# Kernel tuning notes

Hardware: AMD Instinct MI355X
Metric: run time of the kernel (lower is better)

## Reference

```python
import jax, jax.numpy as jnp
import numpy as np

H = 8                 # num_heads
SCALE = 25.0          # self.scale
SIM_THRESH = 0.75
CONF_SIM_THRESH = 0.99


def _l2n(x):
    return x / jnp.linalg.norm(x, axis=-1, keepdims=True)


def setup_inputs() -> dict:
    key = jax.random.key(0)
    ks = jax.random.split(key, 10)
    B, N1, N2, C = 1, 512, 2048, 1024
    s = 0.02
    return {
        'x_cls': jax.random.normal(ks[0], (B, N2, C), jnp.float32),
        'x_reg': jax.random.normal(ks[1], (B, N2, C), jnp.float32),
        'cls_score': jax.random.uniform(ks[2], (N2,), dtype=jnp.float32),
        'fg_score': jax.random.uniform(ks[3], (N2,), dtype=jnp.float32),
        'W_q_cls': jax.random.normal(ks[4], (C, C), jnp.float32) * s,
        'W_kv_cls': jax.random.normal(ks[5], (C, 2 * C), jnp.float32) * s,
        'W_q_reg': jax.random.normal(ks[6], (C, C), jnp.float32) * s,
        'W_kv_reg': jax.random.normal(ks[7], (C, 2 * C), jnp.float32) * s,
        'W_lin': jax.random.normal(ks[8], (2 * C, 2 * C), jnp.float32) * s,
        'b_lin': jnp.zeros((2 * C,), jnp.float32),
        'W_lin_reg': jax.random.normal(ks[9], (2 * C, 2 * C), jnp.float32) * s,
        'b_lin_reg': jnp.zeros((2 * C,), jnp.float32),
        'local_preds_num': 512,
    }


def _forward(x_cls, x_reg, cls_score, fg_score, W_q_cls, W_kv_cls, W_q_reg, W_kv_reg,
             W_lin, b_lin, W_lin_reg, b_lin_reg, N1):
    B, N2, C = x_cls.shape
    hd = C // H
    # QKV projections (torch Linear with bias=False; weights stored [in,out])
    q_cls = (x_cls[:, :N1] @ W_q_cls).reshape(B, N1, H, hd).transpose(0, 2, 1, 3)   # [B,H,N1,hd]
    kv = (x_cls @ W_kv_cls).reshape(B, N2, 2, H, hd).transpose(2, 0, 3, 1, 4)
    k_cls, v_cls = kv[0], kv[1]                                                      # [B,H,N2,hd]
    q_reg = (x_reg[:, :N1] @ W_q_reg).reshape(B, N1, H, hd).transpose(0, 2, 1, 3)
    kv = (x_reg @ W_kv_reg).reshape(B, N2, 2, H, hd).transpose(2, 0, 3, 1, 4)
    k_reg, v_reg = kv[0], kv[1]
    # L2 normalization of q, k and of v for raw similarity
    q_cls, k_cls = _l2n(q_cls), _l2n(k_cls)
    q_reg, k_reg = _l2n(q_reg), _l2n(k_reg)
    v_cls_n, v_reg_n = _l2n(v_cls), _l2n(v_reg)
    # per-key score broadcast over [1,H,N1,N2] (use_mask=False path)
    cs = cls_score.reshape(1, 1, 1, N2)
    # raw value-value similarity
    attn_cls_raw = jnp.einsum('bhqd,bhkd->bhqk', v_cls_n[:, :, :N1], v_cls_n)        # [B,H,N1,N2]
    attn_reg_raw = jnp.einsum('bhqd,bhkd->bhqk', v_reg_n[:, :, :N1], v_reg_n)
    # blended softmax attention (attn_drop=0 -> identity)
    attn_cls = jax.nn.softmax(jnp.einsum('bhqd,bhkd->bhqk', q_cls, k_cls) * SCALE * cs, axis=-1)
    attn_reg = jax.nn.softmax(jnp.einsum('bhqd,bhkd->bhqk', q_reg, k_reg) * SCALE, axis=-1)
    attn = (attn_cls + attn_reg) * 0.5
    # attended features + original local values, then output linears
    x = jnp.einsum('bhqk,bhkd->bhqd', attn, v_cls).transpose(0, 2, 1, 3).reshape(B, N1, C)
    x_ori = v_cls[:, :, :N1].transpose(0, 2, 1, 3).reshape(B, N1, C)
    out_cls = jnp.concatenate([x, x_ori], axis=-1) @ W_lin + b_lin                   # [B,N1,2C]
    xr = jnp.einsum('bhqk,bhkd->bhqd', attn, v_reg).transpose(0, 2, 1, 3).reshape(B, N1, C)
    xr_ori = v_reg[:, :, :N1].transpose(0, 2, 1, 3).reshape(B, N1, C)
    out_reg = jnp.concatenate([xr, xr_ori], axis=-1) @ W_lin_reg + b_lin_reg         # reconf=True
    # ave branch: similarity-masked renormalized second-round averaging (batch 0)
    sim_mask = (attn_cls_raw.sum(axis=1)[0] / H > SIM_THRESH).astype(x_cls.dtype)    # [N1,N2]
    obj_mask = (attn_reg_raw.sum(axis=1)[0] / H > CONF_SIM_THRESH).astype(x_cls.dtype)
    sim_round2 = jax.nn.softmax(attn.sum(axis=1)[0] / H, axis=-1)
    sim_round2 = sim_mask * sim_round2
    sim_round2 = sim_round2 / sim_round2.sum(axis=-1, keepdims=True)
    obj_w = obj_mask * sim_round2
    obj_w = obj_w / obj_w.sum(axis=-1, keepdims=True)
    support_cls = v_cls.transpose(0, 2, 1, 3).reshape(B, N2, C)[0]                   # [N2,C]
    support_reg = v_reg.transpose(0, 2, 1, 3).reshape(B, N2, C)[0]
    cls_feature = jnp.concatenate([sim_round2 @ support_cls, out_cls[0]], axis=-1)   # [N1,3C]
    reg_feature = jnp.concatenate([obj_w @ support_reg, out_reg[0]], axis=-1)        # [N1,3C]
    return cls_feature, reg_feature


def reference(x_cls, x_reg, cls_score, fg_score, W_q_cls, W_kv_cls, W_q_reg, W_kv_reg,
              W_lin, b_lin, W_lin_reg, b_lin_reg, local_preds_num):
    return _forward(x_cls, x_reg, cls_score, fg_score, W_q_cls, W_kv_cls, W_q_reg,
                    W_kv_reg, W_lin, b_lin, W_lin_reg, b_lin_reg, local_preds_num)
```

## Files before the change

kernel.cpp:

```cpp
#include <hip/hip_runtime.h>

typedef _Float16 half8 __attribute__((ext_vector_type(8)));
typedef _Float16 half4v __attribute__((ext_vector_type(4)));
typedef float f32x4 __attribute__((ext_vector_type(4)));

#define GLD16(gptr, lptr) \
    __builtin_amdgcn_global_load_lds((const __attribute__((address_space(1))) void*)(gptr), \
                                     (__attribute__((address_space(3))) void*)(lptr), 16, 0, 0)

#define WAIT_VM3   0x0F73
#define WAIT_VM0   0x0F70
#define WAIT_LGKM0 0xC07F

struct GD {
    const _Float16* A; const _Float16* B; void* C;
    const float* colScale;
    _Float16 *vnp, *vtp, *xop;
    long sAh, sAg, sBh, sBg, sSplit, sCh, sCg;
    int lda, ldb, ldc, K, SK, hmask, hshift;
    int ahx, outHalf, csMode, nx, ny, normMode;
    float alpha;
};

__global__ __launch_bounds__(512, 4)
void hgemm3(GD d0, GD d1, int zSplit)
{
    const bool second = (int)blockIdx.z >= zSplit;
    const GD& d = second ? d1 : d0;
    const int bz = second ? (int)blockIdx.z - zSplit : (int)blockIdx.z;
    const int bx = (int)blockIdx.x, by = (int)blockIdx.y;
    if (bx >= d.nx || by >= d.ny) return;

    __shared__ uint4 smem[4608];
    char* sb = (char*)smem;
    const int tid = threadIdx.x;
    const int w = tid >> 6, l = tid & 63;
    const int m0 = by << 8, n0 = bx << 7;
    const int wm = (w >> 1) << 6, wn = (w & 1) << 6;
    const int kq = l >> 4, lm = l & 15;

    const int zz = bz / d.SK, s = bz - zz * d.SK;
    const int h = d.ahx ? bx : (zz & d.hmask);
    const int g = d.ahx ? zz : (zz >> d.hshift);
    const _Float16* A = d.A + (long)h * d.sAh + (long)g * d.sAg;
    const _Float16* B = d.B + (long)h * d.sBh + (long)g * d.sBg;
    const long Coff = (long)s * d.sSplit + (long)h * d.sCh + (long)g * d.sCg;
    const int kper = d.K / d.SK, kbeg = s * kper;
    const int NT = kper >> 5;

    const int rS = (w << 4) + (l >> 2);
    const int cS = (l & 3) ^ ((l >> 3) & 3);
    const _Float16* gA0 = A + (long)(m0 + rS) * d.lda + kbeg + cS * 8;
    const _Float16* gB0 = B + (long)(n0 + rS) * d.ldb + kbeg + cS * 8;
    const int lo = w * 1024 + l * 16;

    auto stage = [&](int t) {
        char* dst = sb + (t % 3) * 24576;
        GLD16(gA0 + t * 32,                     dst + lo);
        GLD16(gA0 + (long)128 * d.lda + t * 32, dst + 8192 + lo);
        GLD16(gB0 + t * 32,                     dst + 16384 + lo);
    };

    f32x4 acc[4][4] = {};
    stage(0);
    if (NT > 1) stage(1);
    if (NT > 1) __builtin_amdgcn_s_waitcnt(WAIT_VM3);
    else        __builtin_amdgcn_s_waitcnt(WAIT_VM0);
    __builtin_amdgcn_s_barrier();

    const int sw16 = ((kq ^ ((lm >> 1) & 3)) << 4);
    for (int t = 0; t < NT; ++t) {
        const char* cb = sb + (t % 3) * 24576;
        half8 af[4], bfr[4];
        const char* pa = cb + (wm + lm) * 64 + sw16;
        const char* pb = cb + 16384 + (wn + lm) * 64 + sw16;
        #pragma unroll
        for (int i = 0; i < 4; ++i) {
            af[i]  = *(const half8*)(pa + i * 1024);
            bfr[i] = *(const half8*)(pb + i * 1024);
        }
        #pragma unroll
        for (int mi = 0; mi < 4; ++mi)
            #pragma unroll
            for (int ni = 0; ni < 4; ++ni)
                acc[mi][ni] = __builtin_amdgcn_mfma_f32_16x16x32_f16(af[mi], bfr[ni], acc[mi][ni], 0, 0, 0);
        __builtin_amdgcn_s_waitcnt(WAIT_LGKM0);
        if (t + 2 < NT) { stage(t + 2); __builtin_amdgcn_s_waitcnt(WAIT_VM3); }
        else if (t + 1 < NT) __builtin_amdgcn_s_waitcnt(WAIT_VM0);
        __builtin_amdgcn_s_barrier();
    }

    if (d.normMode == 0) {
        const int rbase = m0 + wm + kq * 4;
        #pragma unroll
        for (int mi = 0; mi < 4; ++mi) {
            #pragma unroll
            for (int ni = 0; ni < 4; ++ni) {
                const int col = n0 + wn + ni * 16 + lm;
                float cs = d.alpha;
                if (d.csMode == 1 || (d.csMode == 2 && g == 0)) cs *= d.colScale[col];
                #pragma unroll
                for (int r = 0; r < 4; ++r) {
                    const long row = rbase + mi * 16 + r;
                    const float v = acc[mi][ni][r] * cs;
                    const long off = Coff + row * d.ldc + col;
                    if (d.outHalf) ((_Float16*)d.C)[off] = (_Float16)v;
                    else           ((float*)d.C)[off] = v;
                }
            }
        }
        return;
    }

    float* part = (float*)sb;
    float ssq[4][4];
    #pragma unroll
    for (int mi = 0; mi < 4; ++mi)
        #pragma unroll
        for (int r = 0; r < 4; ++r) {
            float sq = 0.f;
            #pragma unroll
            for (int ni = 0; ni < 4; ++ni) { const float v = acc[mi][ni][r]; sq += v * v; }
            sq += __shfl_xor(sq, 1, 64);
            sq += __shfl_xor(sq, 2, 64);
            sq += __shfl_xor(sq, 4, 64);
            sq += __shfl_xor(sq, 8, 64);
            ssq[mi][r] = sq;
        }
    if (lm == 0) {
        #pragma unroll
        for (int mi = 0; mi < 4; ++mi)
            #pragma unroll
            for (int r = 0; r < 4; ++r)
                part[(w & 1) * 256 + wm + kq * 4 + mi * 16 + r] = ssq[mi][r];
    }
    __syncthreads();

    #pragma unroll
    for (int mi = 0; mi < 4; ++mi) {
        #pragma unroll
        for (int r = 0; r < 4; ++r) {
            const int rl = wm + kq * 4 + mi * 16 + r;
            const float inv = rsqrtf(part[rl] + part[256 + rl]);
            const long rg = m0 + rl;
            if (d.normMode == 1) {
                #pragma unroll
                for (int ni = 0; ni < 4; ++ni) {
                    const int col = n0 + wn + ni * 16 + lm;
                    ((_Float16*)d.C)[(long)g * 524288 + rg * 1024 + col] =
                        (_Float16)(acc[mi][ni][r] * inv);
                }
            } else if (n0 < 1024) {
                #pragma unroll
                for (int ni = 0; ni < 4; ++ni) {
                    const int col = n0 + wn + ni * 16 + lm;
                    ((_Float16*)d.C)[(long)g * 2097152 + rg * 1024 + col] =
                        (_Float16)(acc[mi][ni][r] * inv);
                }
            } else {
                #pragma unroll
                for (int ni = 0; ni < 4; ++ni) {
                    const int nL = n0 - 1024 + wn + ni * 16 + lm;
                    d.vnp[(long)g * 2097152 + rg * 1024 + nL] =
                        (_Float16)(acc[mi][ni][r] * inv);
                    if (rg < 512)
                        d.xop[((long)g * 512 + rg) * 2048 + 1024 + nL] =
                            (_Float16)acc[mi][ni][r];
                }
            }
        }
    }
    if (d.normMode == 2 && n0 >= 1024) {
        #pragma unroll
        for (int mi = 0; mi < 4; ++mi)
            #pragma unroll
            for (int ni = 0; ni < 4; ++ni) {
                const int nL = n0 - 1024 + wn + ni * 16 + lm;
                half4v t;
                t.x = (_Float16)acc[mi][ni][0]; t.y = (_Float16)acc[mi][ni][1];
                t.z = (_Float16)acc[mi][ni][2]; t.w = (_Float16)acc[mi][ni][3];
                *(half4v*)(d.vtp + (long)g * 2097152 + (long)nL * 2048
                           + m0 + wm + kq * 4 + mi * 16) = t;
            }
    }
}

static GD mkgd(const _Float16* A, const _Float16* B, void* C, const float* cscale,
               long sAh, long sAg, long sBh, long sBg, long sSplit, long sCh, long sCg,
               int lda, int ldb, int ldc, int K, int SK, int hmask, int hshift,
               int ahx, int outHalf, int csMode, int nx, int ny, float alpha)
{
    GD d; d.A=A; d.B=B; d.C=C; d.colScale=cscale;
    d.vnp=nullptr; d.vtp=nullptr; d.xop=nullptr;
    d.sAh=sAh; d.sAg=sAg; d.sBh=sBh; d.sBg=sBg; d.sSplit=sSplit; d.sCh=sCh; d.sCg=sCg;
    d.lda=lda; d.ldb=ldb; d.ldc=ldc; d.K=K; d.SK=SK; d.hmask=hmask; d.hshift=hshift;
    d.ahx=ahx; d.outHalf=outHalf; d.csMode=csMode; d.nx=nx; d.ny=ny; d.normMode=0;
    d.alpha=alpha;
    return d;
}

__global__ __launch_bounds__(256)
void prep_all(const float* __restrict__ x_cls, const float* __restrict__ x_reg,
              const float* __restrict__ Wq_c, const float* __restrict__ Wq_r,
              const float* __restrict__ Wkv_c, const float* __restrict__ Wkv_r,
              const float* __restrict__ Wl_c, const float* __restrict__ Wl_r,
              _Float16* __restrict__ xbf,
              _Float16* __restrict__ WqT, _Float16* __restrict__ WkvT,
              _Float16* __restrict__ WlinT)
{
    const int z = blockIdx.z;
    if (z == 6) {
        const int lin = blockIdx.y * 64 + blockIdx.x;
        const int which = lin >> 11;
        const int i = (lin & 2047) * 256 + threadIdx.x;
        const float* s = which ? x_reg : x_cls;
        const float4 v = ((const float4*)s)[i];
        half4v o;
        o.x = (_Float16)v.x; o.y = (_Float16)v.y; o.z = (_Float16)v.z; o.w = (_Float16)v.w;
        ((half4v*)(xbf + (size_t)which * 2097152))[i] = o;
        return;
    }
    __shared__ float t[32][33];
    const float* src; _Float16* dst; int ldsrc, lddst, nx, ky;
    switch (z) {
        case 0: src=Wq_c;  dst=WqT;            ldsrc=1024; lddst=1024; nx=32; ky=32; break;
        case 1: src=Wq_r;  dst=WqT+1048576;    ldsrc=1024; lddst=1024; nx=32; ky=32; break;
        case 2: src=Wkv_c; dst=WkvT;           ldsrc=2048; lddst=1024; nx=64; ky=32; break;
        case 3: src=Wkv_r; dst=WkvT+2097152;   ldsrc=2048; lddst=1024; nx=64; ky=32; break;
        case 4: src=Wl_c;  dst=WlinT;          ldsrc=2048; lddst=2048; nx=64; ky=64; break;
        default:src=Wl_r;  dst=WlinT+4194304;  ldsrc=2048; lddst=2048; nx=64; ky=64; break;
    }
    if ((int)blockIdx.x >= nx || (int)blockIdx.y >= ky) return;
    const int n0 = blockIdx.x << 5, k0 = blockIdx.y << 5;
    const int tx = threadIdx.x & 31, ty = threadIdx.x >> 5;
    #pragma unroll
    for (int j = ty; j < 32; j += 8)
        t[j][tx] = src[(size_t)(k0 + j) * ldsrc + n0 + tx];
    __syncthreads();
    #pragma unroll
    for (int j = ty; j < 32; j += 8)
        dst[(size_t)(n0 + j) * lddst + k0 + tx] = (_Float16)t[tx][j];
}

template<int OP>
__device__ __forceinline__ float bred(float v, float* lds)
{
    #pragma unroll
    for (int o = 32; o > 0; o >>= 1) {
        const float u = __shfl_xor(v, o, 64);
        v = OP ? fmaxf(v, u) : v + u;
    }
    __syncthreads();
    if ((threadIdx.x & 63) == 0) lds[threadIdx.x >> 6] = v;
    __syncthreads();
    return OP ? fmaxf(fmaxf(lds[0], lds[1]), fmaxf(lds[2], lds[3]))
              : lds[0] + lds[1] + lds[2] + lds[3];
}

template<int OP>
__device__ __forceinline__ void bred2(float& a, float& b, float* lds)
{
    #pragma unroll
    for (int o = 32; o > 0; o >>= 1) {
        const float ua = __shfl_xor(a, o, 64);
        const float ub = __shfl_xor(b, o, 64);
        a = OP ? fmaxf(a, ua) : a + ua;
        b = OP ? fmaxf(b, ub) : b + ub;
    }
    __syncthreads();
    if ((threadIdx.x & 63) == 0) {
        const int wi = threadIdx.x >> 6;
        lds[wi] = a; lds[4 + wi] = b;
    }
    __syncthreads();
    a = OP ? fmaxf(fmaxf(lds[0], lds[1]), fmaxf(lds[2], lds[3]))
           : lds[0] + lds[1] + lds[2] + lds[3];
    b = OP ? fmaxf(fmaxf(lds[4], lds[5]), fmaxf(lds[6], lds[7]))
           : lds[4] + lds[5] + lds[6] + lds[7];
}

__global__ __launch_bounds__(256)
void sb2_kernel(const _Float16* __restrict__ S16, const float* __restrict__ simPart,
                _Float16* __restrict__ attn,
                _Float16* __restrict__ wc, _Float16* __restrict__ wr)
{
    __shared__ float lds[8];
    const int q = blockIdx.x, t = threadIdx.x;
    const int c0 = t * 8;
    float asum[8] = {};
    for (int hh = 0; hh < 8; ++hh) {
        const size_t rb = (size_t)(hh * 512 + q) * 2048 + c0;
        const half8 hc = *(const half8*)(S16 + rb);
        const half8 hr = *(const half8*)(S16 + 8388608 + rb);
        float vc[8], vr[8];
        float mc = -1e30f, mr = -1e30f;
        #pragma unroll
        for (int j = 0; j < 8; ++j) {
            vc[j] = (float)hc[j]; vr[j] = (float)hr[j];
            mc = fmaxf(mc, vc[j]); mr = fmaxf(mr, vr[j]);
        }
        bred2<1>(mc, mr, lds);
        float sc = 0.f, sr = 0.f;
        #pragma unroll
        for (int j = 0; j < 8; ++j) {
            vc[j] = expf(vc[j] - mc); sc += vc[j];
            vr[j] = expf(vr[j] - mr); sr += vr[j];
        }
        bred2<0>(sc, sr, lds);
        const float ic = 0.5f / sc, ir = 0.5f / sr;
        half8 oa;
        #pragma unroll
        for (int j = 0; j < 8; ++j) {
            const float a = vc[j] * ic + vr[j] * ir;
            oa[j] = (_Float16)a;
            asum[j] += a;
        }
        *(half8*)(attn + rb) = oa;
    }
    float mx = -1e30f;
    #pragma unroll
    for (int j = 0; j < 8; ++j) { asum[j] *= 0.125f; mx = fmaxf(mx, asum[j]); }
    mx = bred<1>(mx, lds);
    const size_t qb = (size_t)q * 2048 + c0;
    float sim[8], reg[8];
    {
        const float4 a0 = *(const float4*)(simPart + qb);
        const float4 a1 = *(const float4*)(simPart + qb + 4);
        const float4 b0 = *(const float4*)(simPart + 2097152 + qb);
        const float4 b1 = *(const float4*)(simPart + 2097152 + qb + 4);
        sim[0]=a0.x+b0.x; sim[1]=a0.y+b0.y; sim[2]=a0.z+b0.z; sim[3]=a0.w+b0.w;
        sim[4]=a1.x+b1.x; sim[5]=a1.y+b1.y; sim[6]=a1.z+b1.z; sim[7]=a1.w+b1.w;
        const float4 c0_ = *(const float4*)(simPart + 1048576 + qb);
        const float4 c1_ = *(const float4*)(simPart + 1048576 + qb + 4);
        const float4 d0_ = *(const float4*)(simPart + 2097152 + 1048576 + qb);
        const float4 d1_ = *(const float4*)(simPart + 2097152 + 1048576 + qb + 4);
        reg[0]=c0_.x+d0_.x; reg[1]=c0_.y+d0_.y; reg[2]=c0_.z+d0_.z; reg[3]=c0_.w+d0_.w;
        reg[4]=c1_.x+d1_.x; reg[5]=c1_.y+d1_.y; reg[6]=c1_.z+d1_.z; reg[7]=c1_.w+d1_.w;
    }
    float em[8], emo[8];
    float s1 = 0.f, s2 = 0.f;
    #pragma unroll
    for (int j = 0; j < 8; ++j) {
        const float e = expf(asum[j] - mx);
        const float m  = sim[j] > 0.75f ? 1.f : 0.f;
        const float mo = reg[j] > 0.99f ? 1.f : 0.f;
        em[j] = e * m; emo[j] = e * m * mo;
        s1 += em[j]; s2 += emo[j];
    }
    bred2<0>(s1, s2, lds);
    const float i1 = 1.f / s1, i2 = 1.f / s2;
    half8 o1, o2;
    #pragma unroll
    for (int j = 0; j < 8; ++j) {
        o1[j] = (_Float16)(em[j] * i1);
        o2[j] = (_Float16)(emo[j] * i2);
    }
    *(half8*)(wc + qb) = o1;
    *(half8*)(wr + qb) = o2;
}

__global__ __launch_bounds__(256)
void build_xcat(const _Float16* __restrict__ xcatPart, _Float16* __restrict__ xcat)
{
    const int v8 = blockIdx.x * 256 + threadIdx.x;
    const int g = v8 >> 16;
    const int n = (v8 >> 7) & 511;
    const int j = (v8 & 127) * 8;
    const size_t p = (size_t)g * 524288 + (size_t)n * 1024 + j;
    float a[8] = {};
    #pragma unroll
    for (int s = 0; s < 4; ++s) {
        const half8 v = *(const half8*)(xcatPart + (size_t)s * 1048576 + p);
        #pragma unroll
        for (int k = 0; k < 8; ++k) a[k] += (float)v[k];
    }
    half8 o;
    #pragma unroll
    for (int k = 0; k < 8; ++k) o[k] = (_Float16)a[k];
    *(half8*)(xcat + ((size_t)g * 512 + n) * 2048 + j) = o;
}

__global__ __launch_bounds__(256)
void finalize(const float* __restrict__ avePart, const float* __restrict__ outPart,
              const float* __restrict__ b_lin, const float* __restrict__ b_lin_reg,
              float* __restrict__ out)
{
    const int v4 = blockIdx.x * 256 + threadIdx.x;
    const size_t base = (size_t)v4 * 4;
    const int c = (int)(base % 3072);
    const int r = (int)((base / 3072) & 511);
    const int g = (int)(base / (3072 * 512));
    float4 v;
    if (c < 1024) {
        const size_t p = (size_t)g * 524288 + (size_t)r * 1024 + c;
        v = make_float4(0.f, 0.f, 0.f, 0.f);
        #pragma unroll
        for (int s = 0; s < 4; ++s) {
            const float4 u = *(const float4*)(avePart + (size_t)s * 1048576 + p);
            v.x += u.x; v.y += u.y; v.z += u.z; v.w += u.w;
        }
    } else {
        const int cc = c - 1024;
        v = *(const float4*)((g ? b_lin_reg : b_lin) + cc);
        const size_t p = (size_t)g * 1048576 + (size_t)r * 2048 + cc;
        #pragma unroll
        for (int s = 0; s < 4; ++s) {
            const float4 u = *(const float4*)(outPart + (size_t)s * 2097152 + p);
            v.x += u.x; v.y += u.y; v.z += u.z; v.w += u.w;
        }
    }
    *(float4*)(out + base) = v;
}

extern "C" void kernel_launch(void* const* d_in, const int* in_sizes, int n_in,
                              void* d_out, int out_size, void* d_ws, size_t ws_size,
                              hipStream_t stream)
{
    const float* x_cls     = (const float*)d_in[0];
    const float* x_reg     = (const float*)d_in[1];
    const float* cls_score = (const float*)d_in[2];
    const float* W_q_cls   = (const float*)d_in[4];
    const float* W_kv_cls  = (const float*)d_in[5];
    const float* W_q_reg   = (const float*)d_in[6];
    const float* W_kv_reg  = (const float*)d_in[7];
    const float* W_lin     = (const float*)d_in[8];
    const float* b_lin     = (const float*)d_in[9];
    const float* W_lin_reg = (const float*)d_in[10];
    const float* b_lin_reg = (const float*)d_in[11];
    float* out = (float*)d_out;

    if (ws_size < (size_t)124 * 1048576) return;

    char* W = (char*)d_ws;
    auto at = [&](size_t mb) { return (void*)(W + mb * 1048576); };
    _Float16* WlinT   = (_Float16*)at(0);
    _Float16* vT      = (_Float16*)at(16);
    _Float16* w_c     = (_Float16*)at(24);
    _Float16* w_r     = (_Float16*)at(26);
    _Float16* qn      = (_Float16*)at(28);
    _Float16* kn      = (_Float16*)at(30);
    _Float16* vn      = (_Float16*)at(38);
    _Float16* xbf     = (_Float16*)at(46);
    _Float16* WkvT    = (_Float16*)at(54);
    _Float16* WqT     = (_Float16*)at(62);
    _Float16* S16     = (_Float16*)at(66);
    float*    simPart = (float*)at(46);
    _Float16* attn_h  = (_Float16*)at(28);
    float*    avePart = (float*)at(46);
    _Float16* xcatPart= (_Float16*)at(62);
    float*    outPart = (float*)at(70);
    _Float16* xcat16  = (_Float16*)at(102);

    prep_all<<<dim3(64, 64, 7), 256, 0, stream>>>(
        x_cls, x_reg, W_q_cls, W_q_reg, W_kv_cls, W_kv_reg, W_lin, W_lin_reg,
        xbf, WqT, WkvT, WlinT);

    {
        GD q  = mkgd(xbf, WqT, qn, nullptr,
                     0, 2097152, 0, 1048576, 0, 0, 0,
                     1024, 1024, 1024, 1024, 1, 0, 0, 1, 0, 0, 8, 2, 1.f);
        q.normMode = 1;
        GD kv = mkgd(xbf, WkvT, kn, nullptr,
                     0, 2097152, 0, 2097152, 0, 0, 0,
                     1024, 1024, 1024, 1024, 1, 0, 0, 1, 0, 0, 16, 8, 1.f);
        kv.normMode = 2; kv.vnp = vn; kv.vtp = vT; kv.xop = xcat16;
        hgemm3<<<dim3(16, 8, 4), 512, 0, stream>>>(q, kv, 2);
    }

    {
        GD vs = mkgd(vn, vn, simPart, nullptr,
                     0, 2097152, 0, 2097152, 2097152, 0, 1048576,
                     1024, 1024, 2048, 1024, 2, 0, 0, 0, 0, 0, 16, 2, 0.125f);
        GD sc = mkgd(qn, kn, S16, cls_score,
                     128, 524288, 128, 2097152, 0, 1048576, 8388608,
                     1024, 1024, 2048, 128, 1, 7, 3, 0, 1, 2, 16, 2, 25.f);
        hgemm3<<<dim3(16, 2, 20), 512, 0, stream>>>(vs, sc, 4);
    }

    sb2_kernel<<<512, 256, 0, stream>>>(S16, simPart, attn_h, w_c, w_r);

    {
        GD av = mkgd(attn_h, vT, xcatPart, nullptr,
                     1048576, 0, 0, 2097152, 1048576, 0, 524288,
                     2048, 2048, 1024, 2048, 4, 0, 0, 1, 1, 0, 8, 2, 1.f);
        GD ae = mkgd(w_c, vT, avePart, nullptr,
                     0, 1048576, 0, 2097152, 1048576, 0, 524288,
                     2048, 2048, 1024, 2048, 4, 0, 0, 0, 0, 0, 8, 2, 1.f);
        hgemm3<<<dim3(8, 2, 16), 512, 0, stream>>>(av, ae, 8);
    }

    build_xcat<<<512, 256, 0, stream>>>(xcatPart, xcat16);

    {
        GD ol = mkgd(xcat16, WlinT, outPart, nullptr,
                     0, 1048576, 0, 4194304, 2097152, 0, 1048576,
                     2048, 2048, 2048, 2048, 4, 0, 0, 0, 0, 0, 16, 2, 1.f);
        hgemm3<<<dim3(16, 2, 8), 512, 0, stream>>>(ol, ol, 8);
    }

    finalize<<<3072, 256, 0, stream>>>(avePart, outPart, b_lin, b_lin_reg, out);
}
```

Baseline: 271.1 us.

## Replace split-K partial buffers and finalize with atomic adds into output; drop softmax max

The split-K GEMMs for the aggregated-value and output-linear stages now atomically add their partials straight into the final output, which is pre-initialised with zeros and biases inside the prep kernel. This removes the finalize kernel and its read of the partial buffers. Separately, the softmax in sb2 drops the max-subtraction reductions, relying on bounded logits (scale 25 on normalized dot products) so that exp cannot overflow. Atomics add contention and make the summation order nondeterministic.

New measurement: 297.9 us. 9.9% more time.

```diff
diff --git a/kernel.cpp b/kernel.cpp
--- a/kernel.cpp
+++ b/kernel.cpp
@@ -18,7 +18,7 @@
     _Float16 *vnp, *vtp, *xop;
     long sAh, sAg, sBh, sBg, sSplit, sCh, sCg;
     int lda, ldb, ldc, K, SK, hmask, hshift;
-    int ahx, outHalf, csMode, nx, ny, normMode;
+    int ahx, outHalf, csMode, nx, ny, normMode, atomOut;
     float alpha;
 };
 
@@ -104,8 +104,9 @@
                     const long row = rbase + mi * 16 + r;
                     const float v = acc[mi][ni][r] * cs;
                     const long off = Coff + row * d.ldc + col;
-                    if (d.outHalf) ((_Float16*)d.C)[off] = (_Float16)v;
-                    else           ((float*)d.C)[off] = v;
+                    if (d.atomOut)      unsafeAtomicAdd((float*)d.C + off, v);
+                    else if (d.outHalf) ((_Float16*)d.C)[off] = (_Float16)v;
+                    else                ((float*)d.C)[off] = v;
                 }
             }
         }
@@ -195,7 +196,7 @@
     d.sAh=sAh; d.sAg=sAg; d.sBh=sBh; d.sBg=sBg; d.sSplit=sSplit; d.sCh=sCh; d.sCg=sCg;
     d.lda=lda; d.ldb=ldb; d.ldc=ldc; d.K=K; d.SK=SK; d.hmask=hmask; d.hshift=hshift;
     d.ahx=ahx; d.outHalf=outHalf; d.csMode=csMode; d.nx=nx; d.ny=ny; d.normMode=0;
-    d.alpha=alpha;
+    d.atomOut=0; d.alpha=alpha;
     return d;
 }
 
@@ -204,9 +205,10 @@
               const float* __restrict__ Wq_c, const float* __restrict__ Wq_r,
               const float* __restrict__ Wkv_c, const float* __restrict__ Wkv_r,
               const float* __restrict__ Wl_c, const float* __restrict__ Wl_r,
+              const float* __restrict__ b_lin, const float* __restrict__ b_lin_reg,
               _Float16* __restrict__ xbf,
               _Float16* __restrict__ WqT, _Float16* __restrict__ WkvT,
-              _Float16* __restrict__ WlinT)
+              _Float16* __restrict__ WlinT, float* __restrict__ out)
 {
     const int z = blockIdx.z;
     if (z == 6) {
@@ -220,6 +222,18 @@
         ((half4v*)(xbf + (size_t)which * 2097152))[i] = o;
         return;
     }
+    if (z == 7) {
+        const int lin = blockIdx.y * 64 + blockIdx.x;
+        if (lin >= 3072) return;
+        const size_t base = ((size_t)lin * 256 + threadIdx.x) * 4;
+        const int c = (int)(base % 3072);
+        const int g = (int)(base / (3072 * 512));
+        float4 v;
+        if (c < 1024) v = make_float4(0.f, 0.f, 0.f, 0.f);
+        else          v = *(const float4*)((g ? b_lin_reg : b_lin) + (c - 1024));
+        *(float4*)(out + base) = v;
+        return;
+    }
     __shared__ float t[32][33];
     const float* src; _Float16* dst; int ldsrc, lddst, nx, ky;
     switch (z) {
@@ -243,21 +257,6 @@
 }
 
 template<int OP>
-__device__ __forceinline__ float bred(float v, float* lds)
-{
-    #pragma unroll
-    for (int o = 32; o > 0; o >>= 1) {
-        const float u = __shfl_xor(v, o, 64);
-        v = OP ? fmaxf(v, u) : v + u;
-    }
-    __syncthreads();
-    if ((threadIdx.x & 63) == 0) lds[threadIdx.x >> 6] = v;
-    __syncthreads();
-    return OP ? fmaxf(fmaxf(lds[0], lds[1]), fmaxf(lds[2], lds[3]))
-              : lds[0] + lds[1] + lds[2] + lds[3];
-}
-
-template<int OP>
 __device__ __forceinline__ void bred2(float& a, float& b, float* lds)
 {
     #pragma unroll
@@ -293,18 +292,11 @@
         const half8 hc = *(const half8*)(S16 + rb);
         const half8 hr = *(const half8*)(S16 + 8388608 + rb);
         float vc[8], vr[8];
-        float mc = -1e30f, mr = -1e30f;
+        float sc = 0.f, sr = 0.f;
         #pragma unroll
         for (int j = 0; j < 8; ++j) {
-            vc[j] = (float)hc[j]; vr[j] = (float)hr[j];
-            mc = fmaxf(mc, vc[j]); mr = fmaxf(mr, vr[j]);
-        }
-        bred2<1>(mc, mr, lds);
-        float sc = 0.f, sr = 0.f;
-        #pragma unroll
-        for (int j = 0; j < 8; ++j) {
-            vc[j] = expf(vc[j] - mc); sc += vc[j];
-            vr[j] = expf(vr[j] - mr); sr += vr[j];
+            vc[j] = expf((float)hc[j]); sc += vc[j];
+            vr[j] = expf((float)hr[j]); sr += vr[j];
         }
         bred2<0>(sc, sr, lds);
         const float ic = 0.5f / sc, ir = 0.5f / sr;
@@ -317,10 +309,6 @@
         }
         *(half8*)(attn + rb) = oa;
     }
-    float mx = -1e30f;
-    #pragma unroll
-    for (int j = 0; j < 8; ++j) { asum[j] *= 0.125f; mx = fmaxf(mx, asum[j]); }
-    mx = bred<1>(mx, lds);
     const size_t qb = (size_t)q * 2048 + c0;
     float sim[8], reg[8];
     {
@@ -341,7 +329,7 @@
     float s1 = 0.f, s2 = 0.f;
     #pragma unroll
     for (int j = 0; j < 8; ++j) {
-        const float e = expf(asum[j] - mx);
+        const float e = expf(asum[j] * 0.125f);
         const float m  = sim[j] > 0.75f ? 1.f : 0.f;
         const float mo = reg[j] > 0.99f ? 1.f : 0.f;
         em[j] = e * m; emo[j] = e * m * mo;
@@ -378,38 +366,6 @@
     #pragma unroll
     for (int k = 0; k < 8; ++k) o[k] = (_Float16)a[k];
     *(half8*)(xcat + ((size_t)g * 512 + n) * 2048 + j) = o;
-}
-
-__global__ __launch_bounds__(256)
-void finalize(const float* __restrict__ avePart, const float* __restrict__ outPart,
-              const float* __restrict__ b_lin, const float* __restrict__ b_lin_reg,
-              float* __restrict__ out)
-{
-    const int v4 = blockIdx.x * 256 + threadIdx.x;
-    const size_t base = (size_t)v4 * 4;
-    const int c = (int)(base % 3072);
-    const int r = (int)((base / 3072) & 511);
-    const int g = (int)(base / (3072 * 512));
-    float4 v;
-    if (c < 1024) {
-        const size_t p = (size_t)g * 524288 + (size_t)r * 1024 + c;
-        v = make_float4(0.f, 0.f, 0.f, 0.f);
-        #pragma unroll
-        for (int s = 0; s < 4; ++s) {
-            const float4 u = *(const float4*)(avePart + (size_t)s * 1048576 + p);
-            v.x += u.x; v.y += u.y; v.z += u.z; v.w += u.w;
-        }
-    } else {
-        const int cc = c - 1024;
-        v = *(const float4*)((g ? b_lin_reg : b_lin) + cc);
-        const size_t p = (size_t)g * 1048576 + (size_t)r * 2048 + cc;
-        #pragma unroll
-        for (int s = 0; s < 4; ++s) {
-            const float4 u = *(const float4*)(outPart + (size_t)s * 2097152 + p);
-            v.x += u.x; v.y += u.y; v.z += u.z; v.w += u.w;
-        }
-    }
-    *(float4*)(out + base) = v;
 }
 
 extern "C" void kernel_launch(void* const* d_in, const int* in_sizes, int n_in,
@@ -446,14 +402,12 @@
     _Float16* S16     = (_Float16*)at(66);
     float*    simPart = (float*)at(46);
     _Float16* attn_h  = (_Float16*)at(28);
-    float*    avePart = (float*)at(46);
     _Float16* xcatPart= (_Float16*)at(62);
-    float*    outPart = (float*)at(70);
     _Float16* xcat16  = (_Float16*)at(102);
 
-    prep_all<<<dim3(64, 64, 7), 256, 0, stream>>>(
+    prep_all<<<dim3(64, 64, 8), 256, 0, stream>>>(
         x_cls, x_reg, W_q_cls, W_q_reg, W_kv_cls, W_kv_reg, W_lin, W_lin_reg,
-        xbf, WqT, WkvT, WlinT);
+        b_lin, b_lin_reg, xbf, WqT, WkvT, WlinT, out);
 
     {
         GD q  = mkgd(xbf, WqT, qn, nullptr,
@@ -483,20 +437,20 @@
         GD av = mkgd(attn_h, vT, xcatPart, nullptr,
                      1048576, 0, 0, 2097152, 1048576, 0, 524288,
                      2048, 2048, 1024, 2048, 4, 0, 0, 1, 1, 0, 8, 2, 1.f);
-        GD ae = mkgd(w_c, vT, avePart, nullptr,
-                     0, 1048576, 0, 2097152, 1048576, 0, 524288,
-                     2048, 2048, 1024, 2048, 4, 0, 0, 0, 0, 0, 8, 2, 1.f);
+        GD ae = mkgd(w_c, vT, out, nullptr,
+                     0, 1048576, 0, 2097152, 0, 0, 1572864,
+                     2048, 2048, 3072, 2048, 4, 0, 0, 0, 0, 0, 8, 2, 1.f);
+        ae.atomOut = 1;
         hgemm3<<<dim3(8, 2, 16), 512, 0, stream>>>(av, ae, 8);
     }
 
     build_xcat<<<512, 256, 0, stream>>>(xcatPart, xcat16);
 
     {
-        GD ol = mkgd(xcat16, WlinT, outPart, nullptr,
-                     0, 1048576, 0, 4194304, 2097152, 0, 1048576,
-                     2048, 2048, 2048, 2048, 4, 0, 0, 0, 0, 0, 16, 2, 1.f);
+        GD ol = mkgd(xcat16, WlinT, out + 1024, nullptr,
+                     0, 1048576, 0, 4194304, 0, 0, 1572864,
+                     2048, 2048, 3072, 2048, 4, 0, 0, 0, 0, 0, 16, 2, 1.f);
+        ol.atomOut = 1;
         hgemm3<<<dim3(16, 2, 8), 512, 0, stream>>>(ol, ol, 8);
     }
-
-    finalize<<<3072, 256, 0, stream>>>(avePart, outPart, b_lin, b_lin_reg, out);
-}
+}
```
